# Kernel tuning notes

Hardware: AMD Instinct MI355X
Metric: run time of the kernel (lower is better)

## Reference

```python
import jax, jax.numpy as jnp
import numpy as np

N_INST = 8  # max instance id; ids 1..N_INST, 0 = background
MESH_NORM = 1024.0  # from SegmantationLoss._meshgrid


def _meshgrid(H, W):
    y = jnp.arange(H, dtype=jnp.float32) / MESH_NORM
    x = jnp.arange(W, dtype=jnp.float32) / MESH_NORM
    return jnp.stack([jnp.broadcast_to(y[:, None], (H, W)),
                      jnp.broadcast_to(x[None, :], (H, W))], axis=0)  # [2,H,W]


def _lovasz_hinge_batch(logits, labels, delta=1.0):
    """logits, labels: [K,P] float. Returns [K] lovasz hinge losses."""
    signs = 2.0 * labels - 1.0
    errors = delta - logits * signs
    order = jnp.argsort(-errors, axis=1)  # descending
    es = jnp.take_along_axis(errors, order, axis=1)
    gs = jnp.take_along_axis(labels, order, axis=1)
    gts = gs.sum(axis=1, keepdims=True)
    intersection = gts - jnp.cumsum(gs, axis=1)
    union = gts + jnp.cumsum(1.0 - gs, axis=1)
    jac = 1.0 - intersection / union
    grad = jnp.concatenate([jac[:, :1], jac[:, 1:] - jac[:, :-1]], axis=1)
    return (jax.nn.relu(es) * grad).sum(axis=1)


def setup_inputs() -> dict:
    key = jax.random.key(0)
    k1, k2, k3, k4 = jax.random.split(key, 4)
    B, H, W = 4, 512, 1024
    x_vec = jax.random.normal(k1, (B, 2, H, W), dtype=jnp.float32)
    # small scale so psigma = exp(10*ppsigma) stays in a sane range
    x_sigma = jax.random.normal(k2, (B, 2, H, W), dtype=jnp.float32) * 0.03
    x_seed = jax.random.normal(k3, (B, 1, H, W), dtype=jnp.float32)
    t = jax.random.randint(k4, (B, H, W), 0, 9, dtype=jnp.int32)
    return {"x_vec": x_vec, "x_sigma": x_sigma, "x_seed": x_seed, "t": t}


def reference(x_vec, x_sigma, x_seed, t):
    B, _, H, W = x_vec.shape
    mesh = _meshgrid(H, W)

    emb = jnp.tanh(x_vec) + mesh[None]          # [B,2,H,W] spatial embedding
    ppsig = x_sigma                              # [B,2,H,W] pre-pseudo-sigma
    seed = jax.nn.sigmoid(x_seed)[:, 0]          # [B,H,W]

    ids = jnp.arange(1, N_INST + 1, dtype=t.dtype)
    mf = (t[None] == ids[:, None, None, None]).astype(jnp.float32)  # [N,B,H,W]
    cnt = mf.sum(axis=(2, 3))                    # [N,B]
    present = cnt > 0
    safe = jnp.maximum(cnt, 1.0)
    n_present = jnp.maximum(present.sum(axis=0).astype(jnp.float32), 1.0)  # [B]

    # per-instance masked means
    centroid = jnp.einsum('nbhw,bchw->nbc', mf, emb) / safe[..., None]    # [N,B,2]
    inst_pps = jnp.einsum('nbhw,bchw->nbc', mf, ppsig) / safe[..., None]  # [N,B,2]
    psigma = jnp.exp(10.0 * inst_pps)                                     # [N,B,2]

    # gaussian between pixel and instance embedding (l22n)
    diff2 = (emb[None] - centroid[..., None, None]) ** 2                  # [N,B,2,H,W]
    dist = (diff2 * psigma[..., None, None]).sum(axis=2)                  # [N,B,H,W]
    gauss = jnp.exp(-0.5 * dist)                                          # [N,B,H,W]

    # lovasz hinge per instance on logits 2*gauss - 1 over all pixels
    P = H * W
    lov = _lovasz_hinge_batch((2.0 * gauss - 1.0).reshape(N_INST * B, P),
                              mf.reshape(N_INST * B, P)).reshape(N_INST, B)
    lov = jnp.where(present, lov, 0.0)
    lovasz_loss = (lov.sum(axis=0) / n_present).mean()

    # sigma loss: pixel ppsigma -> detached instance mean ppsigma
    sd = (ppsig[None] - jax.lax.stop_gradient(inst_pps)[..., None, None]) ** 2
    sl = (sd.sum(axis=2) * mf).sum(axis=(2, 3)) / safe                    # [N,B]
    sl = jnp.where(present, sl, 0.0)
    sigma_loss = (sl.sum(axis=0) / n_present).mean()

    # seed loss: background -> 0, foreground -> detached gaussian
    bg = (t == 0).astype(jnp.float32)                                     # [B,H,W]
    bg_cnt = jnp.maximum(bg.sum(axis=(1, 2)), 1.0)
    bg_loss = ((seed ** 2) * bg).sum(axis=(1, 2)) / bg_cnt                # [B]
    fg = ((seed[None] - jax.lax.stop_gradient(gauss)) ** 2 * mf).sum(axis=(2, 3)) / safe
    fg = jnp.where(present, fg, 0.0)
    seed_loss = ((bg_loss + fg.sum(axis=0)) /
                 (1.0 + present.sum(axis=0).astype(jnp.float32))).mean()

    return lovasz_loss + sigma_loss + seed_loss
```

## Files before the change

### kernel.cpp

```cpp
#include <hip/hip_runtime.h>
#include <math.h>

#define B 4
#define H 512
#define W 1024
#define P (H*W)
#define NI 8
#define NSEG 32
#define NB 512
#define INV_BW ((float)NB/2.0f)
#define NSTRIP 128
#define STRIP_PX (P/NSTRIP)
#define K1B 512
#define K1PX (P/K1B)

#define D_CENY 0
#define D_CENX 32
#define D_PSY  64
#define D_PSX  96
#define D_CNT  128
#define D_SL   160
#define D_BGL  192
#define OFF_FGP 256
#define OFF_HIST (256 + NI*512)
#define OFF_FOLD (OFF_HIST + NSEG*NSTRIP*NB)
#define OFF_PK1  OFF_HIST

__device__ __forceinline__ float fast_tanh(float x) {
    float e = __expf(2.0f * x);
    return 1.0f - 2.0f / (e + 1.0f);
}
__device__ __forceinline__ float fast_sigmoid(float x) {
    return 1.0f / (1.0f + __expf(-x));
}
template<int CTRL, int RM>
__device__ __forceinline__ float dpp_add(float x) {
    int y = __builtin_amdgcn_update_dpp(0, __float_as_int(x), CTRL, RM, 0xF, true);
    return x + __int_as_float(y);
}
__device__ __forceinline__ float wred(float x) {
    x = dpp_add<0x111, 0xF>(x);
    x = dpp_add<0x112, 0xF>(x);
    x = dpp_add<0x114, 0xF>(x);
    x = dpp_add<0x118, 0xF>(x);
    x = dpp_add<0x142, 0xA>(x);
    x = dpp_add<0x143, 0xC>(x);
    return x;
}

__global__ __launch_bounds__(256) void k1_stats(const float* __restrict__ xv,
                                                const float* __restrict__ xs,
                                                const float* __restrict__ xseed,
                                                const int*  __restrict__ t,
                                                float* __restrict__ pk1) {
    const int b = blockIdx.y, bx = blockIdx.x, tid = threadIdx.x;
    const int lane = tid & 63, wid = tid >> 6;
    const float* xv_y = xv + (size_t)b*2*P;
    const float* xv_x = xv_y + P;
    const float* xs_y = xs + (size_t)b*2*P;
    const float* xs_x = xs_y + P;
    const float* sdp  = xseed + (size_t)b*P;
    const int*   tb   = t + (size_t)b*P;

    float cnt[NI], sey[NI], sex[NI], sgy[NI], sgx[NI], sq[NI];
    #pragma unroll
    for (int n = 0; n < NI; ++n) { cnt[n]=0.f; sey[n]=0.f; sex[n]=0.f; sgy[n]=0.f; sgx[n]=0.f; sq[n]=0.f; }
    float bgc = 0.f, bgs = 0.f;

    int p0 = bx*K1PX + tid*4;
    float4 vy = *(const float4*)(xv_y + p0);
    float4 vx = *(const float4*)(xv_x + p0);
    float4 sy = *(const float4*)(xs_y + p0);
    float4 sx = *(const float4*)(xs_x + p0);
    float4 se = *(const float4*)(sdp + p0);
    int4   tt = *(const int4*)(tb + p0);
    #pragma unroll
    for (int j = 0; j < 4; ++j) {
        int pix = p0 + j;
        float ey = fast_tanh((&vy.x)[j]) + (float)(pix >> 10) * (1.0f/1024.0f);
        float ex = fast_tanh((&vx.x)[j]) + (float)(pix & 1023) * (1.0f/1024.0f);
        float gy = (&sy.x)[j], gx = (&sx.x)[j];
        int tv = (&tt.x)[j];
        if (tv == 0) {
            float s = fast_sigmoid((&se.x)[j]);
            bgc += 1.f; bgs += s*s;
        }
        float q = gy*gy + gx*gx;
        #pragma unroll
        for (int n = 0; n < NI; ++n) {
            float m = (tv == n+1) ? 1.0f : 0.0f;
            cnt[n] += m; sey[n] += m*ey; sex[n] += m*ex;
            sgy[n] += m*gy; sgx[n] += m*gx; sq[n] += m*q;
        }
    }
    __shared__ float sw[4*64];
    #define RED50(val, slot) { float r_ = wred(val); if (lane == 63) sw[wid*64 + (slot)] = r_; }
    #pragma unroll
    for (int n = 0; n < NI; ++n) {
        RED50(cnt[n], n*6+0); RED50(sey[n], n*6+1); RED50(sex[n], n*6+2);
        RED50(sgy[n], n*6+3); RED50(sgx[n], n*6+4); RED50(sq[n],  n*6+5);
    }
    RED50(bgc, 48); RED50(bgs, 49);
    #undef RED50
    __syncthreads();
    if (tid < 50) {
        float s = sw[tid] + sw[64+tid] + sw[128+tid] + sw[192+tid];
        pk1[(size_t)(b*K1B + bx)*64 + tid] = s;
    }
}

__global__ __launch_bounds__(1024) void k2_finalize(float* __restrict__ wsf,
                                                    const float* __restrict__ pk1,
                                                    float* __restrict__ out) {
    const int tid = threadIdx.x;
    __shared__ float part[16*64];
    __shared__ float ssum[4*64];
    const int v = tid & 63, g = tid >> 6;
    const int b = g >> 2, c = g & 3;
    float acc = 0.f;
    const int jbase = b*K1B + c*128;
    #pragma unroll 8
    for (int i = 0; i < 128; ++i) acc += pk1[(size_t)(jbase + i)*64 + v];
    part[g*64 + v] = acc;
    __syncthreads();
    if (tid < 256) {
        int vb = tid & 63, bb = tid >> 6;
        ssum[bb*64+vb] = part[(bb*4+0)*64+vb] + part[(bb*4+1)*64+vb]
                       + part[(bb*4+2)*64+vb] + part[(bb*4+3)*64+vb];
    }
    __syncthreads();
    if (tid < NSEG) {
        int n = tid >> 2, bb = tid & 3;
        float cv  = ssum[bb*64 + n*6+0];
        float sey = ssum[bb*64 + n*6+1];
        float sex = ssum[bb*64 + n*6+2];
        float sgy = ssum[bb*64 + n*6+3];
        float sgx = ssum[bb*64 + n*6+4];
        float sq  = ssum[bb*64 + n*6+5];
        float safe = fmaxf(cv, 1.0f);
        float ipy = sgy/safe, ipx = sgx/safe;
        wsf[D_CENY+tid] = sey/safe;
        wsf[D_CENX+tid] = sex/safe;
        wsf[D_PSY+tid]  = expf(10.0f*ipy);
        wsf[D_PSX+tid]  = expf(10.0f*ipx);
        wsf[D_CNT+tid]  = cv;
        wsf[D_SL+tid]   = sq/safe - (ipy*ipy + ipx*ipx);
    } else if (tid < NSEG + B) {
        int bb = tid - NSEG;
        wsf[D_BGL+bb] = ssum[bb*64+49] / fmaxf(ssum[bb*64+48], 1.0f);
    } else if (tid == 40) {
        out[0] = 0.f;
    }
}

__global__ __launch_bounds__(512) void k3_hist(const float* __restrict__ xv,
                                               const float* __restrict__ xseed,
                                               const int*  __restrict__ t,
                                               const float* __restrict__ wsf,
                                               unsigned* __restrict__ hist_g,
                                               float* __restrict__ fgp) {
    const int strip = blockIdx.x;
    const int b     = blockIdx.y;
    const int tid   = threadIdx.x;
    const int lane  = tid & 63;

    __shared__ unsigned hist[NI*NB];
    {
        uint4 z = {0u,0u,0u,0u};
        #pragma unroll
        for (int i = 0; i < 2; ++i) *((uint4*)hist + i*512 + tid) = z;
    }
    __shared__ float spar[4*NI];
    if (tid < 4*NI) {
        int n = tid & (NI-1), q = tid >> 3;
        spar[tid] = wsf[q*32 + n*B + b];
    }
    __syncthreads();

    float ceny[NI], cenx[NI], psy[NI], psx[NI], fgn[NI];
    #pragma unroll
    for (int n = 0; n < NI; ++n) {
        ceny[n] = spar[n]; cenx[n] = spar[NI+n];
        psy[n] = spar[2*NI+n]; psx[n] = spar[3*NI+n];
        fgn[n] = 0.f;
    }

    const float* xv_y = xv + (size_t)b*2*P;
    const float* xv_x = xv_y + P;
    const float* sdp  = xseed + (size_t)b*P;
    const int*   tb   = t + (size_t)b*P;
    const int base = strip * STRIP_PX;

    #pragma unroll
    for (int it = 0; it < STRIP_PX/2048; ++it) {
        int p0 = base + it*2048 + tid*4;
        float4 vy = *(const float4*)(xv_y + p0);
        float4 vx = *(const float4*)(xv_x + p0);
        float4 se = *(const float4*)(sdp + p0);
        int4   tt = *(const int4*)(tb + p0);
        #pragma unroll
        for (int j = 0; j < 4; ++j) {
            int pix = p0 + j;
            float ey = fast_tanh((&vy.x)[j]) + (float)(pix >> 10) * (1.0f/1024.0f);
            float ex = fast_tanh((&vx.x)[j]) + (float)(pix & 1023) * (1.0f/1024.0f);
            int tv = (&tt.x)[j];
            float gown = 0.f;
            #pragma unroll
            for (int n = 0; n < NI; ++n) {
                float dy = ey - ceny[n], dx = ex - cenx[n];
                float g = __expf(-0.5f * (psy[n]*dy*dy + psx[n]*dx*dx));
                bool lab = (tv == n+1);
                float err = lab ? (2.0f - 2.0f*g) : (2.0f*g);
                int key = (int)(err * INV_BW);
                key = key > (NB-1) ? (NB-1) : key;
                if (key > 0) atomicAdd(&hist[n*NB + key], lab ? 0x10000u : 1u);
                if (lab) gown = g;
            }
            if (tv > 0) {
                float s = fast_sigmoid((&se.x)[j]);
                float d = s - gown;
                float dd = d*d;
                #pragma unroll
                for (int n = 0; n < NI; ++n) fgn[n] += (tv == n+1) ? dd : 0.f;
            }
        }
    }
    __syncthreads();
    #pragma unroll
    for (int i = 0; i < 2; ++i) {
        int lin = i*2048 + tid*4;
        int n = lin >> 9, key = lin & (NB-1);
        uint4 v = *(const uint4*)&hist[lin];
        *(uint4*)&hist_g[((size_t)((n*4 + b)*NSTRIP + strip))*NB + key] = v;
    }
    __shared__ float sfg[NI];
    if (tid < NI) sfg[tid] = 0.f;
    __syncthreads();
    #pragma unroll
    for (int n = 0; n < NI; ++n) {
        float r = wred(fgn[n]);
        if (lane == 63 && r != 0.f) atomicAdd(&sfg[n], r);
    }
    __syncthreads();
    if (tid < NI) fgp[tid*512 + b*NSTRIP + strip] = sfg[tid];
}

__global__ __launch_bounds__(256) void k4a_fold(const unsigned* __restrict__ hist_g,
                                                unsigned* __restrict__ fold) {
    const int q   = blockIdx.x;
    const int seg = blockIdx.y;
    const int tid = threadIdx.x;
    #pragma unroll
    for (int h = 0; h < 2; ++h) {
        int key = h*256 + tid;
        const unsigned* src = hist_g + (size_t)(seg*NSTRIP + q*32)*NB + key;
        unsigned pos = 0u, neg = 0u;
        #pragma unroll 8
        for (int s = 0; s < 32; ++s) {
            unsigned v = src[(size_t)s*NB];
            pos += v >> 16; neg += v & 0xffffu;
        }
        fold[((size_t)q*NSEG + seg)*NB + key] = pos;
        fold[(size_t)4*NSEG*NB + ((size_t)q*NSEG + seg)*NB + key] = neg;
    }
}

__global__ __launch_bounds__(256) void k4b_scan(const unsigned* __restrict__ fold,
                                                const float* __restrict__ wsf,
                                                const float* __restrict__ fgp,
                                                float* __restrict__ out) {
    const int seg = blockIdx.x, tid = threadIdx.x;
    const int n = seg >> 2, b = seg & 3;
    __shared__ float scnt[NSEG];
    if (tid < NSEG) scnt[tid] = wsf[D_CNT + tid];
    __syncthreads();

    if (seg == 0 && tid == 0) {
        float add = 0.f;
        for (int bb = 0; bb < B; ++bb) {
            int np = 0; float ss = 0.f;
            for (int k = 0; k < NI; ++k) {
                float c = scnt[k*4 + bb];
                if (c > 0.5f) { np++; ss += wsf[D_SL + k*4 + bb]; }
            }
            float npf = fmaxf((float)np, 1.0f);
            add += ss/npf + wsf[D_BGL+bb] / (1.0f + (float)np);
        }
        atomicAdd(out, add * (1.0f/(float)B));
    }

    const float G = scnt[seg];
    if (G < 0.5f) return;
    int npc = 0;
    #pragma unroll
    for (int k = 0; k < NI; ++k) npc += (scnt[k*4 + b] > 0.5f) ? 1 : 0;

    __shared__ float sfr[128];
    if (tid < 128) sfr[tid] = fgp[n*512 + b*NSTRIP + tid];
    __syncthreads();
    #pragma unroll
    for (int d = 64; d > 0; d >>= 1) {
        if (tid < d) sfr[tid] += sfr[tid + d];
        __syncthreads();
    }
    const float FG = sfr[0];

    unsigned pos2[2] = {0u,0u}, neg2[2] = {0u,0u};
    #pragma unroll
    for (int q = 0; q < 4; ++q) {
        uint2 pv = *((const uint2*)(fold + ((size_t)q*NSEG + seg)*NB) + tid);
        uint2 nv = *((const uint2*)(fold + (size_t)4*NSEG*NB + ((size_t)q*NSEG + seg)*NB) + tid);
        pos2[0] += pv.x; pos2[1] += pv.y;
        neg2[0] += nv.x; neg2[1] += nv.y;
    }
    unsigned tp = pos2[0] + pos2[1];
    unsigned tn = neg2[0] + neg2[1];

    __shared__ unsigned up[256], un[256];
    up[tid] = tp; un[tid] = tn;
    __syncthreads();
    for (int d = 1; d < 256; d <<= 1) {
        unsigned ap = (tid + d < 256) ? up[tid + d] : 0u;
        unsigned an = (tid + d < 256) ? un[tid + d] : 0u;
        __syncthreads();
        up[tid] += ap; un[tid] += an;
        __syncthreads();
    }
    const unsigned TP = up[0], TN = un[0];
    const unsigned Gu = (unsigned)(G + 0.5f);
    const unsigned NEGu = (unsigned)P - Gu;
    unsigned cump = up[tid] - tp;
    unsigned cumn = un[tid] - tn;

    const double dG = (double)G;
    double acc = 0.0;
    #pragma unroll
    for (int j = 1; j >= 0; --j) {
        unsigned cp = pos2[j], cn = neg2[j];
        int key = tid*2 + j;
        if (tid == 0 && j == 0) { cp = Gu - TP; cn = NEGu - TN; }
        if (cp | cn) {
            unsigned ep = cump, en = cumn;
            unsigned epi = ep + cp, eni = en + cn;
            double jb = 1.0 - (dG - (double)ep)  / (dG + (double)en);
            double ja = 1.0 - (dG - (double)epi) / (dG + (double)eni);
            acc += (((double)key + 0.5) * (2.0/(double)NB)) * (ja - jb);
        }
        cump += cp; cumn += cn;
    }
    __shared__ double sdd[256];
    sdd[tid] = acc;
    __syncthreads();
    #pragma unroll
    for (int d = 128; d > 0; d >>= 1) {
        if (tid < d) sdd[tid] += sdd[tid + d];
        __syncthreads();
    }
    if (tid == 0) {
        float npf = fmaxf((float)npc, 1.0f);
        float val = (float)sdd[0] / (npf * (float)B)
                  + (FG / G) / ((1.0f + (float)npc) * (float)B);
        atomicAdd(out, val);
    }
}

extern "C" void kernel_launch(void* const* d_in, const int* in_sizes, int n_in,
                              void* d_out, int out_size, void* d_ws, size_t ws_size,
                              hipStream_t stream) {
    (void)in_sizes; (void)n_in; (void)out_size; (void)ws_size;
    const float* xv  = (const float*)d_in[0];
    const float* xs  = (const float*)d_in[1];
    const float* xsd = (const float*)d_in[2];
    const int*   t   = (const int*)d_in[3];
    float* wsf = (float*)d_ws;
    unsigned* hist_g = (unsigned*)d_ws + OFF_HIST;
    unsigned* fold   = (unsigned*)d_ws + OFF_FOLD;
    float* pk1 = wsf + OFF_PK1;
    float* fgp = wsf + OFF_FGP;
    float* out = (float*)d_out;

    k1_stats<<<dim3(K1B, B), 256, 0, stream>>>(xv, xs, xsd, t, pk1);
    k2_finalize<<<1, 1024, 0, stream>>>(wsf, pk1, out);
    k3_hist<<<dim3(NSTRIP, B), 512, 0, stream>>>(xv, xsd, t, wsf, hist_g, fgp);
    k4a_fold<<<dim3(4, NSEG), 256, 0, stream>>>(hist_g, fold);
    k4b_scan<<<NSEG, 256, 0, stream>>>(fold, wsf, fgp, out);
}
```

Baseline: 132.9 us.

## Fuse fold and scan via last-block counter, move bg seed loss to hist kernel

Merges the fold and scan kernels into one launch: each fold block bumps a per-segment atomic counter and the last of the four blocks runs the scan and loss. The background seed statistics move from the stats kernel into the histogram kernel, which already reads the seed, so the stats kernel no longer reads x_seed. The background count is derived as P minus the instance counts. The stats kernel also uses fewer blocks that each process four chunks. This removes a kernel launch and one full pass over the seed input, but adds atomics and fences plus a serial tail on the last-arriving block.

```diff
diff --git a/kernel.cpp b/kernel.cpp
--- a/kernel.cpp
+++ b/kernel.cpp
@@ -11,7 +11,7 @@
 #define INV_BW ((float)NB/2.0f)
 #define NSTRIP 128
 #define STRIP_PX (P/NSTRIP)
-#define K1B 512
+#define K1B 128
 #define K1PX (P/K1B)
 
 #define D_CENY 0
@@ -20,9 +20,9 @@
 #define D_PSX  96
 #define D_CNT  128
 #define D_SL   160
-#define D_BGL  192
+#define D_K4C  192
 #define OFF_FGP 256
-#define OFF_HIST (256 + NI*512)
+#define OFF_HIST (256 + 9*512)
 #define OFF_FOLD (OFF_HIST + NSEG*NSTRIP*NB)
 #define OFF_PK1  OFF_HIST
 
@@ -50,7 +50,6 @@
 
 __global__ __launch_bounds__(256) void k1_stats(const float* __restrict__ xv,
                                                 const float* __restrict__ xs,
-                                                const float* __restrict__ xseed,
                                                 const int*  __restrict__ t,
                                                 float* __restrict__ pk1) {
     const int b = blockIdx.y, bx = blockIdx.x, tid = threadIdx.x;
@@ -59,51 +58,46 @@
     const float* xv_x = xv_y + P;
     const float* xs_y = xs + (size_t)b*2*P;
     const float* xs_x = xs_y + P;
-    const float* sdp  = xseed + (size_t)b*P;
     const int*   tb   = t + (size_t)b*P;
 
     float cnt[NI], sey[NI], sex[NI], sgy[NI], sgx[NI], sq[NI];
     #pragma unroll
     for (int n = 0; n < NI; ++n) { cnt[n]=0.f; sey[n]=0.f; sex[n]=0.f; sgy[n]=0.f; sgx[n]=0.f; sq[n]=0.f; }
-    float bgc = 0.f, bgs = 0.f;
-
-    int p0 = bx*K1PX + tid*4;
-    float4 vy = *(const float4*)(xv_y + p0);
-    float4 vx = *(const float4*)(xv_x + p0);
-    float4 sy = *(const float4*)(xs_y + p0);
-    float4 sx = *(const float4*)(xs_x + p0);
-    float4 se = *(const float4*)(sdp + p0);
-    int4   tt = *(const int4*)(tb + p0);
-    #pragma unroll
-    for (int j = 0; j < 4; ++j) {
-        int pix = p0 + j;
-        float ey = fast_tanh((&vy.x)[j]) + (float)(pix >> 10) * (1.0f/1024.0f);
-        float ex = fast_tanh((&vx.x)[j]) + (float)(pix & 1023) * (1.0f/1024.0f);
-        float gy = (&sy.x)[j], gx = (&sx.x)[j];
-        int tv = (&tt.x)[j];
-        if (tv == 0) {
-            float s = fast_sigmoid((&se.x)[j]);
-            bgc += 1.f; bgs += s*s;
-        }
-        float q = gy*gy + gx*gx;
+
+    #pragma unroll
+    for (int it = 0; it < 4; ++it) {
+        int p0 = bx*K1PX + it*1024 + tid*4;
+        float4 vy = *(const float4*)(xv_y + p0);
+        float4 vx = *(const float4*)(xv_x + p0);
+        float4 sy = *(const float4*)(xs_y + p0);
+        float4 sx = *(const float4*)(xs_x + p0);
+        int4   tt = *(const int4*)(tb + p0);
         #pragma unroll
-        for (int n = 0; n < NI; ++n) {
-            float m = (tv == n+1) ? 1.0f : 0.0f;
-            cnt[n] += m; sey[n] += m*ey; sex[n] += m*ex;
-            sgy[n] += m*gy; sgx[n] += m*gx; sq[n] += m*q;
+        for (int j = 0; j < 4; ++j) {
+            int pix = p0 + j;
+            float ey = fast_tanh((&vy.x)[j]) + (float)(pix >> 10) * (1.0f/1024.0f);
+            float ex = fast_tanh((&vx.x)[j]) + (float)(pix & 1023) * (1.0f/1024.0f);
+            float gy = (&sy.x)[j], gx = (&sx.x)[j];
+            int tv = (&tt.x)[j];
+            float q = gy*gy + gx*gx;
+            #pragma unroll
+            for (int n = 0; n < NI; ++n) {
+                float m = (tv == n+1) ? 1.0f : 0.0f;
+                cnt[n] += m; sey[n] += m*ey; sex[n] += m*ex;
+                sgy[n] += m*gy; sgx[n] += m*gx; sq[n] += m*q;
+            }
         }
     }
     __shared__ float sw[4*64];
-    #define RED50(val, slot) { float r_ = wred(val); if (lane == 63) sw[wid*64 + (slot)] = r_; }
+    #define RED48(val, slot) { float r_ = wred(val); if (lane == 63) sw[wid*64 + (slot)] = r_; }
     #pragma unroll
     for (int n = 0; n < NI; ++n) {
-        RED50(cnt[n], n*6+0); RED50(sey[n], n*6+1); RED50(sex[n], n*6+2);
-        RED50(sgy[n], n*6+3); RED50(sgx[n], n*6+4); RED50(sq[n],  n*6+5);
-    }
-    RED50(bgc, 48); RED50(bgs, 49);
-    #undef RED50
-    __syncthreads();
-    if (tid < 50) {
+        RED48(cnt[n], n*6+0); RED48(sey[n], n*6+1); RED48(sex[n], n*6+2);
+        RED48(sgy[n], n*6+3); RED48(sgx[n], n*6+4); RED48(sq[n],  n*6+5);
+    }
+    #undef RED48
+    __syncthreads();
+    if (tid < 48) {
         float s = sw[tid] + sw[64+tid] + sw[128+tid] + sw[192+tid];
         pk1[(size_t)(b*K1B + bx)*64 + tid] = s;
     }
@@ -118,9 +112,9 @@
     const int v = tid & 63, g = tid >> 6;
     const int b = g >> 2, c = g & 3;
     float acc = 0.f;
-    const int jbase = b*K1B + c*128;
+    const int jbase = b*K1B + c*32;
     #pragma unroll 8
-    for (int i = 0; i < 128; ++i) acc += pk1[(size_t)(jbase + i)*64 + v];
+    for (int i = 0; i < 32; ++i) acc += pk1[(size_t)(jbase + i)*64 + v];
     part[g*64 + v] = acc;
     __syncthreads();
     if (tid < 256) {
@@ -145,10 +139,9 @@
         wsf[D_PSX+tid]  = expf(10.0f*ipx);
         wsf[D_CNT+tid]  = cv;
         wsf[D_SL+tid]   = sq/safe - (ipy*ipy + ipx*ipx);
-    } else if (tid < NSEG + B) {
-        int bb = tid - NSEG;
-        wsf[D_BGL+bb] = ssum[bb*64+49] / fmaxf(ssum[bb*64+48], 1.0f);
-    } else if (tid == 40) {
+    } else if (tid < 64) {
+        ((unsigned*)wsf)[D_K4C + (tid - 32)] = 0u;
+    } else if (tid == 64) {
         out[0] = 0.f;
     }
 }
@@ -184,6 +177,7 @@
         psy[n] = spar[2*NI+n]; psx[n] = spar[3*NI+n];
         fgn[n] = 0.f;
     }
+    float bgq = 0.f;
 
     const float* xv_y = xv + (size_t)b*2*P;
     const float* xv_x = xv_y + P;
@@ -216,12 +210,14 @@
                 if (key > 0) atomicAdd(&hist[n*NB + key], lab ? 0x10000u : 1u);
                 if (lab) gown = g;
             }
+            float s = fast_sigmoid((&se.x)[j]);
             if (tv > 0) {
-                float s = fast_sigmoid((&se.x)[j]);
                 float d = s - gown;
                 float dd = d*d;
                 #pragma unroll
                 for (int n = 0; n < NI; ++n) fgn[n] += (tv == n+1) ? dd : 0.f;
+            } else {
+                bgq += s*s;
             }
         }
     }
@@ -233,23 +229,31 @@
         uint4 v = *(const uint4*)&hist[lin];
         *(uint4*)&hist_g[((size_t)((n*4 + b)*NSTRIP + strip))*NB + key] = v;
     }
-    __shared__ float sfg[NI];
-    if (tid < NI) sfg[tid] = 0.f;
+    __shared__ float sfg[NI+1];
+    if (tid < NI+1) sfg[tid] = 0.f;
     __syncthreads();
     #pragma unroll
     for (int n = 0; n < NI; ++n) {
         float r = wred(fgn[n]);
         if (lane == 63 && r != 0.f) atomicAdd(&sfg[n], r);
     }
-    __syncthreads();
-    if (tid < NI) fgp[tid*512 + b*NSTRIP + strip] = sfg[tid];
-}
-
-__global__ __launch_bounds__(256) void k4a_fold(const unsigned* __restrict__ hist_g,
-                                                unsigned* __restrict__ fold) {
-    const int q   = blockIdx.x;
+    {
+        float r = wred(bgq);
+        if (lane == 63) atomicAdd(&sfg[NI], r);
+    }
+    __syncthreads();
+    if (tid < NI+1) fgp[tid*512 + b*NSTRIP + strip] = sfg[tid];
+}
+
+__global__ __launch_bounds__(256) void k4_fused(const unsigned* __restrict__ hist_g,
+                                                unsigned* __restrict__ fold,
+                                                float* __restrict__ wsf,
+                                                const float* __restrict__ fgp,
+                                                float* __restrict__ out) {
+    const int q = blockIdx.x;
     const int seg = blockIdx.y;
     const int tid = threadIdx.x;
+
     #pragma unroll
     for (int h = 0; h < 2; ++h) {
         int key = h*256 + tid;
@@ -263,30 +267,49 @@
         fold[((size_t)q*NSEG + seg)*NB + key] = pos;
         fold[(size_t)4*NSEG*NB + ((size_t)q*NSEG + seg)*NB + key] = neg;
     }
-}
-
-__global__ __launch_bounds__(256) void k4b_scan(const unsigned* __restrict__ fold,
-                                                const float* __restrict__ wsf,
-                                                const float* __restrict__ fgp,
-                                                float* __restrict__ out) {
-    const int seg = blockIdx.x, tid = threadIdx.x;
+
+    __shared__ unsigned slast;
+    __syncthreads();
+    if (tid == 0) {
+        __threadfence();
+        unsigned* cnt4 = (unsigned*)wsf + D_K4C;
+        slast = __hip_atomic_fetch_add(&cnt4[seg], 1u, __ATOMIC_ACQ_REL,
+                                       __HIP_MEMORY_SCOPE_AGENT);
+    }
+    __syncthreads();
+    if (slast != 3u) return;
+    __threadfence();
+
     const int n = seg >> 2, b = seg & 3;
     __shared__ float scnt[NSEG];
+    __shared__ float sfr[128];
+    __shared__ unsigned up[256], un[256];
+    __shared__ double sdd[256];
     if (tid < NSEG) scnt[tid] = wsf[D_CNT + tid];
     __syncthreads();
 
-    if (seg == 0 && tid == 0) {
-        float add = 0.f;
-        for (int bb = 0; bb < B; ++bb) {
-            int np = 0; float ss = 0.f;
+    if (n == 0) {
+        if (tid < 128) sfr[tid] = fgp[NI*512 + b*NSTRIP + tid];
+        __syncthreads();
+        #pragma unroll
+        for (int d = 64; d > 0; d >>= 1) {
+            if (tid < d) sfr[tid] += sfr[tid + d];
+            __syncthreads();
+        }
+        if (tid == 0) {
+            float bgs = sfr[0];
+            int np = 0; float ss = 0.f, csum = 0.f;
             for (int k = 0; k < NI; ++k) {
-                float c = scnt[k*4 + bb];
-                if (c > 0.5f) { np++; ss += wsf[D_SL + k*4 + bb]; }
+                float cv = scnt[k*4 + b];
+                csum += cv;
+                if (cv > 0.5f) { np++; ss += wsf[D_SL + k*4 + b]; }
             }
+            float bgc = fmaxf((float)P - csum, 1.0f);
+            float bgl = bgs / bgc;
             float npf = fmaxf((float)np, 1.0f);
-            add += ss/npf + wsf[D_BGL+bb] / (1.0f + (float)np);
-        }
-        atomicAdd(out, add * (1.0f/(float)B));
+            atomicAdd(out, (ss/npf + bgl/(1.0f + (float)np)) * (1.0f/(float)B));
+        }
+        __syncthreads();
     }
 
     const float G = scnt[seg];
@@ -295,7 +318,6 @@
     #pragma unroll
     for (int k = 0; k < NI; ++k) npc += (scnt[k*4 + b] > 0.5f) ? 1 : 0;
 
-    __shared__ float sfr[128];
     if (tid < 128) sfr[tid] = fgp[n*512 + b*NSTRIP + tid];
     __syncthreads();
     #pragma unroll
@@ -307,16 +329,15 @@
 
     unsigned pos2[2] = {0u,0u}, neg2[2] = {0u,0u};
     #pragma unroll
-    for (int q = 0; q < 4; ++q) {
-        uint2 pv = *((const uint2*)(fold + ((size_t)q*NSEG + seg)*NB) + tid);
-        uint2 nv = *((const uint2*)(fold + (size_t)4*NSEG*NB + ((size_t)q*NSEG + seg)*NB) + tid);
+    for (int qq = 0; qq < 4; ++qq) {
+        uint2 pv = *((const uint2*)(fold + ((size_t)qq*NSEG + seg)*NB) + tid);
+        uint2 nv = *((const uint2*)(fold + (size_t)4*NSEG*NB + ((size_t)qq*NSEG + seg)*NB) + tid);
         pos2[0] += pv.x; pos2[1] += pv.y;
         neg2[0] += nv.x; neg2[1] += nv.y;
     }
     unsigned tp = pos2[0] + pos2[1];
     unsigned tn = neg2[0] + neg2[1];
 
-    __shared__ unsigned up[256], un[256];
     up[tid] = tp; un[tid] = tn;
     __syncthreads();
     for (int d = 1; d < 256; d <<= 1) {
@@ -348,7 +369,6 @@
         }
         cump += cp; cumn += cn;
     }
-    __shared__ double sdd[256];
     sdd[tid] = acc;
     __syncthreads();
     #pragma unroll
@@ -379,9 +399,8 @@
     float* fgp = wsf + OFF_FGP;
     float* out = (float*)d_out;
 
-    k1_stats<<<dim3(K1B, B), 256, 0, stream>>>(xv, xs, xsd, t, pk1);
+    k1_stats<<<dim3(K1B, B), 256, 0, stream>>>(xv, xs, t, pk1);
     k2_finalize<<<1, 1024, 0, stream>>>(wsf, pk1, out);
     k3_hist<<<dim3(NSTRIP, B), 512, 0, stream>>>(xv, xsd, t, wsf, hist_g, fgp);
-    k4a_fold<<<dim3(4, NSEG), 256, 0, stream>>>(hist_g, fold);
-    k4b_scan<<<NSEG, 256, 0, stream>>>(fold, wsf, fgp, out);
-}
+    k4_fused<<<dim3(4, NSEG), 256, 0, stream>>>(hist_g, fold, wsf, fgp, out);
+}
```

Result: faster. 128.0 us (-3.7%).
